# Optimization experiments

Hardware: AMD Instinct MI355X
Metric: run time of the kernel (lower is better)

## Reference

```python
import jax, jax.numpy as jnp
import numpy as np

H = 4          # hidden_size
NUM_LAYERS = 5
SEQ = 610
BATCH = 128


def _lstm_layer(x, w_i, w_h, bi, bh):
    # x: [B, T, I]; w_i: [4H, I]; w_h: [4H, H]; bi, bh: [4H]
    # PyTorch gate order: i, f, g, o
    B = x.shape[0]
    b = bi + bh

    def step(carry, xt):
        h, c = carry
        gates = xt @ w_i.T + h @ w_h.T + b          # [B, 4H]
        i, f, g, o = jnp.split(gates, 4, axis=-1)
        c = jax.nn.sigmoid(f) * c + jax.nn.sigmoid(i) * jnp.tanh(g)
        h = jax.nn.sigmoid(o) * jnp.tanh(c)
        return (h, c), h

    h0 = jnp.zeros((B, H), x.dtype)
    c0 = jnp.zeros((B, H), x.dtype)
    (_, _), hs = jax.lax.scan(step, (h0, c0), jnp.swapaxes(x, 0, 1))  # hs: [T, B, H]
    return jnp.swapaxes(hs, 0, 1)                   # [B, T, H]


def setup_inputs() -> dict:
    key = jax.random.key(0)
    ks = jax.random.split(key, 10)
    s = 1.0 / np.sqrt(H)  # PyTorch default uniform(-1/sqrt(H), 1/sqrt(H))
    u = lambda k, shape: jax.random.uniform(k, shape, jnp.float32, -s, s)
    return {
        "x": jax.random.normal(ks[0], (BATCH, SEQ, 2), jnp.float32),
        "w_ih0": u(ks[1], (4 * H, 2)),
        "w_ih": u(ks[2], (NUM_LAYERS - 1, 4 * H, H)),
        "w_hh": u(ks[3], (NUM_LAYERS, 4 * H, H)),
        "b_ih": u(ks[4], (NUM_LAYERS, 4 * H)),
        "b_hh": u(ks[5], (NUM_LAYERS, 4 * H)),
        "w_lin": u(ks[6], (1, H)),
        "b_lin": u(ks[7], (1,)),
        "w_fc": jax.random.uniform(ks[8], (5, SEQ), jnp.float32, -1.0 / np.sqrt(SEQ), 1.0 / np.sqrt(SEQ)),
        "b_fc": jax.random.uniform(ks[9], (5,), jnp.float32, -1.0 / np.sqrt(SEQ), 1.0 / np.sqrt(SEQ)),
    }


def reference(x, w_ih0, w_ih, w_hh, b_ih, b_hh, w_lin, b_lin, w_fc, b_fc):
    # 5-layer stacked LSTM, zero initial state (as on the module's first call)
    out = _lstm_layer(x, w_ih0, w_hh[0], b_ih[0], b_hh[0])
    for l in range(NUM_LAYERS - 1):
        out = _lstm_layer(out, w_ih[l], w_hh[l + 1], b_ih[l + 1], b_hh[l + 1])
    # per-timestep Linear(4 -> 1) then cat along dim 1 -> [B, T]
    t = (out @ w_lin.T + b_lin)[..., 0]             # [B, 610]
    return t @ w_fc.T + b_fc                         # [B, 5]
```

## Files before the change

### kernel.cpp

```cpp
#include <hip/hip_runtime.h>
#include <math.h>

#define H 4
#define NL 5
#define SEQ 610
#define BATCH 128
#define NITER 619
#define HEAD 16
#define TAIL0 616

typedef float v2f __attribute__((ext_vector_type(2)));

#if __has_builtin(__builtin_elementwise_fma)
#define FMA2(a, b, c) __builtin_elementwise_fma((a), (b), (c))
#else
static __device__ __forceinline__ v2f FMA2(v2f a, v2f b, v2f c) {
    v2f r; r[0] = fmaf(a[0], b[0], c[0]); r[1] = fmaf(a[1], b[1], c[1]); return r;
}
#endif

static __device__ __forceinline__ v2f splat2(float a) { v2f r; r[0] = a; r[1] = a; return r; }

template<int CTRL, bool BC>
__device__ __forceinline__ float dpp1(float old_, float src) {
    return __int_as_float(__builtin_amdgcn_update_dpp(
        __float_as_int(old_), __float_as_int(src), CTRL, 0xF, 0xF, BC));
}

__global__ __launch_bounds__(64) void lstm_pk_kernel(
    const float* __restrict__ x,
    const float* __restrict__ w_ih0,
    const float* __restrict__ w_ih,
    const float* __restrict__ w_hh,
    const float* __restrict__ b_ih,
    const float* __restrict__ b_hh,
    const float* __restrict__ w_lin,
    const float* __restrict__ b_lin,
    const float* __restrict__ w_fc,
    const float* __restrict__ b_fc,
    float* __restrict__ out)
{
    __shared__ float lds_x[2 * SEQ * 2 + 32];
    __shared__ float lds_wfcp[4 * SEQ * 2 + 8];

    const int lane = threadIdx.x;
    const int half = lane >> 5;
    const int r    = lane & 31;
    const int l    = r >> 2;
    const int k    = r & 3;
    const int lw   = l > 4 ? 4 : l;
    const bool is_l0 = (l == 0);
    const int row  = blockIdx.x * 2 + half;

    #pragma unroll
    for (int hh = 0; hh < 2; ++hh) {
        const float4* src = (const float4*)(x + (size_t)(blockIdx.x * 2 + hh) * (SEQ * 2));
        float4* dst = (float4*)&lds_x[hh * (SEQ * 2)];
        for (int i = lane; i < (SEQ * 2) / 4; i += 64) dst[i] = src[i];
    }
    #pragma unroll
    for (int kk = 0; kk < 4; ++kk) {
        for (int t = lane; t < SEQ; t += 64) {
            lds_wfcp[(kk * SEQ + t) * 2 + 0] = w_fc[kk * SEQ + t];
            lds_wfcp[(kk * SEQ + t) * 2 + 1] = w_fc[4 * SEQ + t];
        }
    }
    __syncthreads();

    v2f wip01[4], wip23[4], whp01[4], whp23[4], b01, b23;
    {
        float wi[4][4], wh[4][4], bias[4];
        #pragma unroll
        for (int j = 0; j < 4; ++j) {
            const float s = (j == 2) ? 2.8853900817779268f
                                     : -1.4426950408889634f;
            const int wrow = j * H + k;
            if (lw == 0) {
                wi[j][0] = w_ih0[wrow * 2 + 0] * s;
                wi[j][1] = w_ih0[wrow * 2 + 1] * s;
                wi[j][2] = 0.f; wi[j][3] = 0.f;
            } else {
                const float4 v = *(const float4*)&w_ih[((lw - 1) * 16 + wrow) * 4];
                wi[j][0] = v.x * s; wi[j][1] = v.y * s; wi[j][2] = v.z * s; wi[j][3] = v.w * s;
            }
            const float4 u = *(const float4*)&w_hh[(lw * 16 + wrow) * 4];
            wh[j][0] = u.x * s; wh[j][1] = u.y * s; wh[j][2] = u.z * s; wh[j][3] = u.w * s;
            bias[j] = (b_ih[lw * 16 + wrow] + b_hh[lw * 16 + wrow]) * s;
        }
        #pragma unroll
        for (int m = 0; m < 4; ++m) {
            wip01[m][0] = wi[0][m]; wip01[m][1] = wi[1][m];
            wip23[m][0] = wi[2][m]; wip23[m][1] = wi[3][m];
            whp01[m][0] = wh[0][m]; whp01[m][1] = wh[1][m];
            whp23[m][0] = wh[2][m]; whp23[m][1] = wh[3][m];
        }
        b01[0] = bias[0]; b01[1] = bias[1];
        b23[0] = bias[2]; b23[1] = bias[3];
    }
    const float wl0 = w_lin[0], wl1 = w_lin[1], wl2 = w_lin[2], wl3 = w_lin[3];
    const float bl  = b_lin[0];

    const int xb     = half * (SEQ * 2);
    const int wpbase = k * SEQ;

    float c = 0.f;
    float q0 = 0.f, q1 = 0.f, q2 = 0.f, q3 = 0.f;
    float accA = 0.f, accB = 0.f;
    v2f pre01, pre23;
    {
        const float2 xv0 = *(const float2*)&lds_x[xb];
        const float xs0 = is_l0 ? xv0.x : 0.f;
        const float xs1 = is_l0 ? xv0.y : 0.f;
        pre01 = FMA2(wip01[1], splat2(xs1), FMA2(wip01[0], splat2(xs0), b01));
        pre23 = FMA2(wip23[1], splat2(xs1), FMA2(wip23[0], splat2(xs0), b23));
    }

    #define TICK_CORE(tau_, GATED, NXv, WVv)                                          \
    {                                                                                 \
        const float oq0 = q0, oq1 = q1, oq2 = q2, oq3 = q3;                           \
                             \
        v2f G01 = FMA2(whp01[3], splat2(oq3), FMA2(whp01[2], splat2(oq2),             \
                  FMA2(whp01[1], splat2(oq1), FMA2(whp01[0], splat2(oq0), pre01)))); \
        v2f G23 = FMA2(whp23[3], splat2(oq3), FMA2(whp23[2], splat2(oq2),             \
                  FMA2(whp23[1], splat2(oq1), FMA2(whp23[0], splat2(oq0), pre23)))); \
        const float Ai = 1.f + __builtin_amdgcn_exp2f(G01[0]);                        \
        const float Af = 1.f + __builtin_amdgcn_exp2f(G01[1]);                        \
        const float Dg = 1.f + __builtin_amdgcn_exp2f(G23[0]);                        \
        const float Ao = 1.f + __builtin_amdgcn_exp2f(G23[1]);                        \
        const float M   = Ai * Dg;                                                    \
        const float den = M * Af;                                                     \
        const float num = fmaf(c, M, Af * (Dg - 2.f));                                \
        float cn = num * __builtin_amdgcn_rcpf(den);                                  \
        if (GATED) { const unsigned tt = (unsigned)((tau_) - 2 * l);                  \
                     cn = (tt < SEQ) ? cn : 0.f; }                                    \
        c = cn;                                                                       \
        const float Dc = 1.f + __builtin_amdgcn_exp2f(c * 2.8853900817779268f);       \
        const float hv = (Dc - 2.f) * __builtin_amdgcn_rcpf(Ao * Dc);                 \
        q0 = dpp1<0x00, true>(0.f, hv);                                               \
        q1 = dpp1<0x55, true>(0.f, hv);                                               \
        q2 = dpp1<0xAA, true>(0.f, hv);                                               \
        q3 = dpp1<0xFF, true>(0.f, hv);                                               \
                               \
        float p0 = dpp1<0x142, true>(0.f, oq0); p0 = dpp1<0x114, false>(p0, oq0);     \
        float p1 = dpp1<0x142, true>(0.f, oq1); p1 = dpp1<0x114, false>(p1, oq1);     \
        float p2 = dpp1<0x142, true>(0.f, oq2); p2 = dpp1<0x114, false>(p2, oq2);     \
        float p3 = dpp1<0x142, true>(0.f, oq3); p3 = dpp1<0x114, false>(p3, oq3);     \
        const float xs0 = is_l0 ? (NXv).x : p0;                                       \
        const float xs1 = is_l0 ? (NXv).y : p1;                                       \
        pre01 = FMA2(wip01[3], splat2(p3), FMA2(wip01[2], splat2(p2),                 \
                FMA2(wip01[1], splat2(xs1), FMA2(wip01[0], splat2(xs0), b01))));      \
        pre23 = FMA2(wip23[3], splat2(p3), FMA2(wip23[2], splat2(p2),                 \
                FMA2(wip23[1], splat2(xs1), FMA2(wip23[0], splat2(xs0), b23))));      \
        float tval = fmaf(oq0, wl0, fmaf(oq1, wl1, fmaf(oq2, wl2, fmaf(oq3, wl3, bl)))); \
        if (GATED) tval = ((unsigned)((tau_) - 9) < SEQ) ? tval : 0.f;                \
        accA = fmaf(tval, (WVv).x, accA);                                             \
        accB = fmaf(tval, (WVv).y, accB);                                             \
    }

    for (int tau = 0; tau < HEAD; ++tau) {
        const float2 nx = *(const float2*)&lds_x[xb + (tau + 1) * 2];
        int t4 = tau - 9; t4 = t4 < 0 ? 0 : t4;
        const float2 wv = *(const float2*)&lds_wfcp[(wpbase + t4) * 2];
        TICK_CORE(tau, true, nx, wv);
    }

    for (int ch = 0; ch < 75; ++ch) {
        const int tau0 = HEAD + ch * 8;
        float2 xc[8], wc[8];
        #pragma unroll
        for (int i = 0; i < 8; ++i) {
            xc[i] = *(const float2*)&lds_x[xb + (tau0 + 1 + i) * 2];
            wc[i] = *(const float2*)&lds_wfcp[(wpbase + tau0 + i - 9) * 2];
        }
        #pragma unroll
        for (int i = 0; i < 8; ++i) {
            TICK_CORE(tau0 + i, false, xc[i], wc[i]);
        }
    }

    for (int tau = TAIL0; tau < NITER; ++tau) {
        const float2 nx = *(const float2*)&lds_x[xb + (tau + 1) * 2];
        const float2 wv = *(const float2*)&lds_wfcp[(wpbase + tau - 9) * 2];
        TICK_CORE(tau, true, nx, wv);
    }
    #undef TICK_CORE

    if (r >= 16 && r < 20) {
        out[row * 5 + k] = accA + b_fc[k];
        if (k == 0) out[row * 5 + 4] = accB + b_fc[4];
    }
}

extern "C" void kernel_launch(void* const* d_in, const int* in_sizes, int n_in,
                              void* d_out, int out_size, void* d_ws, size_t ws_size,
                              hipStream_t stream)
{
    const float* x     = (const float*)d_in[0];
    const float* w_ih0 = (const float*)d_in[1];
    const float* w_ih  = (const float*)d_in[2];
    const float* w_hh  = (const float*)d_in[3];
    const float* b_ih  = (const float*)d_in[4];
    const float* b_hh  = (const float*)d_in[5];
    const float* w_lin = (const float*)d_in[6];
    const float* b_lin = (const float*)d_in[7];
    const float* w_fc  = (const float*)d_in[8];
    const float* b_fc  = (const float*)d_in[9];
    float* out = (float*)d_out;

    lstm_pk_kernel<<<dim3(BATCH / 2), dim3(64), 0, stream>>>(
        x, w_ih0, w_ih, w_hh, b_ih, b_hh, w_lin, b_lin, w_fc, b_fc, out);
}
```

Before: 158.9 us.

## Split gate pairs across lanes, one batch row per wavefront

Each wavefront now handles one batch row instead of two. Each unit (layer, k) is spread over two lanes, each computing two of the four gates as a packed pair, and DPP row shifts exchange the gate activations between partner lanes. The grid doubles to 128 blocks, which halves the FMA chain per lane in the serial recurrence. In exchange, extra DPP ops sit on the critical path (now three per layer input instead of two) and more wavefronts are launched.

```diff
diff --git a/kernel.cpp b/kernel.cpp
--- a/kernel.cpp
+++ b/kernel.cpp
@@ -18,16 +18,15 @@
     v2f r; r[0] = fmaf(a[0], b[0], c[0]); r[1] = fmaf(a[1], b[1], c[1]); return r;
 }
 #endif
-
 static __device__ __forceinline__ v2f splat2(float a) { v2f r; r[0] = a; r[1] = a; return r; }
 
-template<int CTRL, bool BC>
-__device__ __forceinline__ float dpp1(float old_, float src) {
+template<int CTRL, int RM, int BM, bool BC>
+__device__ __forceinline__ float dppm(float old_, float src) {
     return __int_as_float(__builtin_amdgcn_update_dpp(
-        __float_as_int(old_), __float_as_int(src), CTRL, 0xF, 0xF, BC));
-}
-
-__global__ __launch_bounds__(64) void lstm_pk_kernel(
+        __float_as_int(old_), __float_as_int(src), CTRL, RM, BM, BC));
+}
+
+__global__ __launch_bounds__(64) void lstm_jk_kernel(
     const float* __restrict__ x,
     const float* __restrict__ w_ih0,
     const float* __restrict__ w_ih,
@@ -40,22 +39,20 @@
     const float* __restrict__ b_fc,
     float* __restrict__ out)
 {
-    __shared__ float lds_x[2 * SEQ * 2 + 32];
+    __shared__ float lds_x[SEQ * 2 + 32];
     __shared__ float lds_wfcp[4 * SEQ * 2 + 8];
 
-    const int lane = threadIdx.x;
-    const int half = lane >> 5;
-    const int r    = lane & 31;
-    const int l    = r >> 2;
-    const int k    = r & 3;
-    const int lw   = l > 4 ? 4 : l;
-    const bool is_l0 = (l == 0);
-    const int row  = blockIdx.x * 2 + half;
-
-    #pragma unroll
-    for (int hh = 0; hh < 2; ++hh) {
-        const float4* src = (const float4*)(x + (size_t)(blockIdx.x * 2 + hh) * (SEQ * 2));
-        float4* dst = (float4*)&lds_x[hh * (SEQ * 2)];
+    const int lane  = threadIdx.x;
+    const int l_raw = lane >> 3;
+    const int l     = l_raw > 4 ? 4 : l_raw;
+    const int j2    = (lane >> 2) & 1;
+    const int k     = lane & 3;
+    const bool is_l0 = (l_raw == 0);
+    const int b     = blockIdx.x;
+
+    {
+        const float4* src = (const float4*)(x + (size_t)b * (SEQ * 2));
+        float4* dst = (float4*)lds_x;
         for (int i = lane; i < (SEQ * 2) / 4; i += 64) dst[i] = src[i];
     }
     #pragma unroll
@@ -67,98 +64,96 @@
     }
     __syncthreads();
 
-    v2f wip01[4], wip23[4], whp01[4], whp23[4], b01, b23;
+    v2f wip[4], whp[4], bp;
     {
-        float wi[4][4], wh[4][4], bias[4];
-        #pragma unroll
-        for (int j = 0; j < 4; ++j) {
-            const float s = (j == 2) ? 2.8853900817779268f
-                                     : -1.4426950408889634f;
-            const int wrow = j * H + k;
-            if (lw == 0) {
-                wi[j][0] = w_ih0[wrow * 2 + 0] * s;
-                wi[j][1] = w_ih0[wrow * 2 + 1] * s;
-                wi[j][2] = 0.f; wi[j][3] = 0.f;
-            } else {
-                const float4 v = *(const float4*)&w_ih[((lw - 1) * 16 + wrow) * 4];
-                wi[j][0] = v.x * s; wi[j][1] = v.y * s; wi[j][2] = v.z * s; wi[j][3] = v.w * s;
-            }
-            const float4 u = *(const float4*)&w_hh[(lw * 16 + wrow) * 4];
-            wh[j][0] = u.x * s; wh[j][1] = u.y * s; wh[j][2] = u.z * s; wh[j][3] = u.w * s;
-            bias[j] = (b_ih[lw * 16 + wrow] + b_hh[lw * 16 + wrow]) * s;
-        }
+        const int ga = 2 * j2, gb = 2 * j2 + 1;
+        const float sa = (ga == 2) ? 2.8853900817779268f : -1.4426950408889634f;
+        const float sb = -1.4426950408889634f;
+        const int ra = ga * H + k, rb = gb * H + k;
         #pragma unroll
         for (int m = 0; m < 4; ++m) {
-            wip01[m][0] = wi[0][m]; wip01[m][1] = wi[1][m];
-            wip23[m][0] = wi[2][m]; wip23[m][1] = wi[3][m];
-            whp01[m][0] = wh[0][m]; whp01[m][1] = wh[1][m];
-            whp23[m][0] = wh[2][m]; whp23[m][1] = wh[3][m];
-        }
-        b01[0] = bias[0]; b01[1] = bias[1];
-        b23[0] = bias[2]; b23[1] = bias[3];
+            float wa, wb;
+            if (l == 0) {
+                wa = (m < 2) ? w_ih0[ra * 2 + m] : 0.f;
+                wb = (m < 2) ? w_ih0[rb * 2 + m] : 0.f;
+            } else {
+                wa = w_ih[((l - 1) * 16 + ra) * 4 + m];
+                wb = w_ih[((l - 1) * 16 + rb) * 4 + m];
+            }
+            wip[m][0] = wa * sa; wip[m][1] = wb * sb;
+            whp[m][0] = w_hh[(l * 16 + ra) * 4 + m] * sa;
+            whp[m][1] = w_hh[(l * 16 + rb) * 4 + m] * sb;
+        }
+        bp[0] = (b_ih[l * 16 + ra] + b_hh[l * 16 + ra]) * sa;
+        bp[1] = (b_ih[l * 16 + rb] + b_hh[l * 16 + rb]) * sb;
     }
     const float wl0 = w_lin[0], wl1 = w_lin[1], wl2 = w_lin[2], wl3 = w_lin[3];
     const float bl  = b_lin[0];
-
-    const int xb     = half * (SEQ * 2);
     const int wpbase = k * SEQ;
 
     float c = 0.f;
     float q0 = 0.f, q1 = 0.f, q2 = 0.f, q3 = 0.f;
-    float accA = 0.f, accB = 0.f;
-    v2f pre01, pre23;
+    v2f acc2 = splat2(0.f);
+    v2f pre;
     {
-        const float2 xv0 = *(const float2*)&lds_x[xb];
+        const float2 xv0 = *(const float2*)&lds_x[0];
         const float xs0 = is_l0 ? xv0.x : 0.f;
         const float xs1 = is_l0 ? xv0.y : 0.f;
-        pre01 = FMA2(wip01[1], splat2(xs1), FMA2(wip01[0], splat2(xs0), b01));
-        pre23 = FMA2(wip23[1], splat2(xs1), FMA2(wip23[0], splat2(xs0), b23));
+        pre = FMA2(wip[1], splat2(xs1), FMA2(wip[0], splat2(xs0), bp));
     }
 
     #define TICK_CORE(tau_, GATED, NXv, WVv)                                          \
     {                                                                                 \
         const float oq0 = q0, oq1 = q1, oq2 = q2, oq3 = q3;                           \
-                             \
-        v2f G01 = FMA2(whp01[3], splat2(oq3), FMA2(whp01[2], splat2(oq2),             \
-                  FMA2(whp01[1], splat2(oq1), FMA2(whp01[0], splat2(oq0), pre01)))); \
-        v2f G23 = FMA2(whp23[3], splat2(oq3), FMA2(whp23[2], splat2(oq2),             \
-                  FMA2(whp23[1], splat2(oq1), FMA2(whp23[0], splat2(oq0), pre23)))); \
-        const float Ai = 1.f + __builtin_amdgcn_exp2f(G01[0]);                        \
-        const float Af = 1.f + __builtin_amdgcn_exp2f(G01[1]);                        \
-        const float Dg = 1.f + __builtin_amdgcn_exp2f(G23[0]);                        \
-        const float Ao = 1.f + __builtin_amdgcn_exp2f(G23[1]);                        \
-        const float M   = Ai * Dg;                                                    \
-        const float den = M * Af;                                                     \
-        const float num = fmaf(c, M, Af * (Dg - 2.f));                                \
+                               \
+        v2f G = FMA2(whp[3], splat2(oq3), FMA2(whp[2], splat2(oq2),                   \
+                FMA2(whp[1], splat2(oq1), FMA2(whp[0], splat2(oq0), pre))));          \
+        v2f E; E[0] = __builtin_amdgcn_exp2f(G[0]);                                   \
+        E[1] = __builtin_amdgcn_exp2f(G[1]);                                          \
+        v2f A = E + 1.f;                            \
+        v2f X, Y;                              \
+        X[0] = dppm<0x114, 0xF, 0xA, false>(A[0], A[0]);                              \
+        X[1] = dppm<0x114, 0xF, 0xA, false>(A[1], A[1]);                              \
+        Y[0] = dppm<0x104, 0xF, 0x5, false>(A[0], A[0]);                              \
+        Y[1] = dppm<0x104, 0xF, 0x5, false>(A[1], A[1]);                              \
+        const float M   = X[0] * Y[0];                                                \
+        const float den = M * X[1];                                                   \
+        const float num = fmaf(c, M, X[1] * (Y[0] - 2.f));                            \
         float cn = num * __builtin_amdgcn_rcpf(den);                                  \
-        if (GATED) { const unsigned tt = (unsigned)((tau_) - 2 * l);                  \
+        if (GATED) { const unsigned tt = (unsigned)((tau_) - 2 * l_raw);              \
                      cn = (tt < SEQ) ? cn : 0.f; }                                    \
         c = cn;                                                                       \
         const float Dc = 1.f + __builtin_amdgcn_exp2f(c * 2.8853900817779268f);       \
-        const float hv = (Dc - 2.f) * __builtin_amdgcn_rcpf(Ao * Dc);                 \
-        q0 = dpp1<0x00, true>(0.f, hv);                                               \
-        q1 = dpp1<0x55, true>(0.f, hv);                                               \
-        q2 = dpp1<0xAA, true>(0.f, hv);                                               \
-        q3 = dpp1<0xFF, true>(0.f, hv);                                               \
-                               \
-        float p0 = dpp1<0x142, true>(0.f, oq0); p0 = dpp1<0x114, false>(p0, oq0);     \
-        float p1 = dpp1<0x142, true>(0.f, oq1); p1 = dpp1<0x114, false>(p1, oq1);     \
-        float p2 = dpp1<0x142, true>(0.f, oq2); p2 = dpp1<0x114, false>(p2, oq2);     \
-        float p3 = dpp1<0x142, true>(0.f, oq3); p3 = dpp1<0x114, false>(p3, oq3);     \
+        const float hv = (Dc - 2.f) * __builtin_amdgcn_rcpf(Y[1] * Dc);               \
+        q0 = dppm<0x00, 0xF, 0xF, true>(0.f, hv);                                     \
+        q1 = dppm<0x55, 0xF, 0xF, true>(0.f, hv);                                     \
+        q2 = dppm<0xAA, 0xF, 0xF, true>(0.f, hv);                                     \
+        q3 = dppm<0xFF, 0xF, 0xF, true>(0.f, hv);                                     \
+                  \
+        float p0 = dppm<0x118, 0xF, 0xF, true>(0.f, oq0);                             \
+        p0 = dppm<0x142, 0x2, 0x3, false>(p0, oq0);                                   \
+        p0 = dppm<0x143, 0x4, 0x3, false>(p0, oq0);                                   \
+        float p1 = dppm<0x118, 0xF, 0xF, true>(0.f, oq1);                             \
+        p1 = dppm<0x142, 0x2, 0x3, false>(p1, oq1);                                   \
+        p1 = dppm<0x143, 0x4, 0x3, false>(p1, oq1);                                   \
+        float p2 = dppm<0x118, 0xF, 0xF, true>(0.f, oq2);                             \
+        p2 = dppm<0x142, 0x2, 0x3, false>(p2, oq2);                                   \
+        p2 = dppm<0x143, 0x4, 0x3, false>(p2, oq2);                                   \
+        float p3 = dppm<0x118, 0xF, 0xF, true>(0.f, oq3);                             \
+        p3 = dppm<0x142, 0x2, 0x3, false>(p3, oq3);                                   \
+        p3 = dppm<0x143, 0x4, 0x3, false>(p3, oq3);                                   \
         const float xs0 = is_l0 ? (NXv).x : p0;                                       \
         const float xs1 = is_l0 ? (NXv).y : p1;                                       \
-        pre01 = FMA2(wip01[3], splat2(p3), FMA2(wip01[2], splat2(p2),                 \
-                FMA2(wip01[1], splat2(xs1), FMA2(wip01[0], splat2(xs0), b01))));      \
-        pre23 = FMA2(wip23[3], splat2(p3), FMA2(wip23[2], splat2(p2),                 \
-                FMA2(wip23[1], splat2(xs1), FMA2(wip23[0], splat2(xs0), b23))));      \
+        pre = FMA2(wip[3], splat2(p3), FMA2(wip[2], splat2(p2),                       \
+              FMA2(wip[1], splat2(xs1), FMA2(wip[0], splat2(xs0), bp))));             \
         float tval = fmaf(oq0, wl0, fmaf(oq1, wl1, fmaf(oq2, wl2, fmaf(oq3, wl3, bl)))); \
         if (GATED) tval = ((unsigned)((tau_) - 9) < SEQ) ? tval : 0.f;                \
-        accA = fmaf(tval, (WVv).x, accA);                                             \
-        accB = fmaf(tval, (WVv).y, accB);                                             \
+        v2f wvv; wvv[0] = (WVv).x; wvv[1] = (WVv).y;                                  \
+        acc2 = FMA2(splat2(tval), wvv, acc2);                                         \
     }
 
     for (int tau = 0; tau < HEAD; ++tau) {
-        const float2 nx = *(const float2*)&lds_x[xb + (tau + 1) * 2];
+        const float2 nx = *(const float2*)&lds_x[(tau + 1) * 2];
         int t4 = tau - 9; t4 = t4 < 0 ? 0 : t4;
         const float2 wv = *(const float2*)&lds_wfcp[(wpbase + t4) * 2];
         TICK_CORE(tau, true, nx, wv);
@@ -166,28 +161,28 @@
 
     for (int ch = 0; ch < 75; ++ch) {
         const int tau0 = HEAD + ch * 8;
-        float2 xc[8], wc[8];
+        float2 xc_[8], wc_[8];
         #pragma unroll
         for (int i = 0; i < 8; ++i) {
-            xc[i] = *(const float2*)&lds_x[xb + (tau0 + 1 + i) * 2];
-            wc[i] = *(const float2*)&lds_wfcp[(wpbase + tau0 + i - 9) * 2];
+            xc_[i] = *(const float2*)&lds_x[(tau0 + 1 + i) * 2];
+            wc_[i] = *(const float2*)&lds_wfcp[(wpbase + tau0 + i - 9) * 2];
         }
         #pragma unroll
         for (int i = 0; i < 8; ++i) {
-            TICK_CORE(tau0 + i, false, xc[i], wc[i]);
+            TICK_CORE(tau0 + i, false, xc_[i], wc_[i]);
         }
     }
 
     for (int tau = TAIL0; tau < NITER; ++tau) {
-        const float2 nx = *(const float2*)&lds_x[xb + (tau + 1) * 2];
+        const float2 nx = *(const float2*)&lds_x[(tau + 1) * 2];
         const float2 wv = *(const float2*)&lds_wfcp[(wpbase + tau - 9) * 2];
         TICK_CORE(tau, true, nx, wv);
     }
     #undef TICK_CORE
 
-    if (r >= 16 && r < 20) {
-        out[row * 5 + k] = accA + b_fc[k];
-        if (k == 0) out[row * 5 + 4] = accB + b_fc[4];
+    if (lane >= 32 && lane < 36) {
+        out[b * 5 + k] = acc2[0] + b_fc[k];
+        if (k == 0) out[b * 5 + 4] = acc2[1] + b_fc[4];
     }
 }
 
@@ -207,6 +202,6 @@
     const float* b_fc  = (const float*)d_in[9];
     float* out = (float*)d_out;
 
-    lstm_pk_kernel<<<dim3(BATCH / 2), dim3(64), 0, stream>>>(
+    lstm_jk_kernel<<<dim3(BATCH), dim3(64), 0, stream>>>(
         x, w_ih0, w_ih, w_hh, b_ih, b_hh, w_lin, b_lin, w_fc, b_fc, out);
 }
```

Result: no change. 157.0 us (-1.2%).
